# Performance work log

Hardware: AMD Instinct MI355X
Metric: run time of the kernel (lower is better)

Reference implementation:

```python
import jax, jax.numpy as jnp
import numpy as np

HIDDEN = 1024
HEADS = 16


def rotate_half(x):
    x1, x2 = jnp.split(x, 2, axis=-1)
    return jnp.concatenate((-x2, x1), axis=-1)


def rope_tables(seq_len, dim):
    inv_freq = 1.0 / 10000 ** (jnp.arange(0, dim, 2, dtype=jnp.float32) / dim)
    t = jnp.arange(seq_len, dtype=jnp.float32)
    freqs = jnp.outer(t, inv_freq)
    emb = jnp.concatenate((freqs, freqs), axis=-1)  # [S, dim]
    return jnp.cos(emb), jnp.sin(emb)


def setup_inputs() -> dict:
    key = jax.random.key(0)
    ks = jax.random.split(key, 10)
    B, S, D = 2, 2048, HIDDEN
    scale = 1.0 / np.sqrt(D)
    inp = {
        "inputs": jax.random.normal(ks[0], (B, S, D), jnp.float32),
        "context": jax.random.normal(ks[1], (B, S, D), jnp.float32),
        "Wq": jax.random.normal(ks[2], (D, D), jnp.float32) * scale,
        "bq": jnp.zeros((D,), jnp.float32),
        "Wk": jax.random.normal(ks[3], (D, D), jnp.float32) * scale,
        "bk": jnp.zeros((D,), jnp.float32),
        "Wv": jax.random.normal(ks[4], (D, D), jnp.float32) * scale,
        "bv": jnp.zeros((D,), jnp.float32),
        "Wo": jax.random.normal(ks[5], (D, D), jnp.float32) * scale,
        "bo": jnp.zeros((D,), jnp.float32),
    }
    return inp


def reference(inputs, context, Wq, bq, Wk, bk, Wv, bv, Wo, bo):
    B, S, D = inputs.shape
    H = HEADS
    hd = D // H

    q = inputs @ Wq + bq          # [B,S,D]
    k = context @ Wk + bk
    v = context @ Wv + bv

    # RoPE applied over the FULL hidden dim, pre-head-split (faithful to source).
    cos, sin = rope_tables(S, D)  # [S,D]
    # source indexes [0] after broadcasting with [1,1,S,D] tables -> effectively same values
    q = q * cos + rotate_half(q) * sin
    k = k * cos + rotate_half(k) * sin

    q = q.reshape(B, S, H, hd)
    k = k.reshape(B, S, H, hd)
    v = v.reshape(B, S, H, hd)

    # Faithful: NO transpose before attention; matmul contracts last dims of
    # q [B,S,H,hd] with k^T [B,S,hd,H] -> scores [B,S,H,H]
    scores = jnp.einsum('bshd,btd->bsht', q, jnp.zeros((1, 1, 1))) if False else None
    scores = jnp.matmul(q, jnp.swapaxes(k, -2, -1)) / jnp.sqrt(jnp.float32(hd))  # [B,S,H,H]
    attn = jax.nn.softmax(scores, axis=-1)
    ctx = jnp.matmul(attn, v)     # [B,S,H,hd]

    # source: transpose(0,2,1,3) then reshape back to (B,S,D)
    ctx = ctx.transpose(0, 2, 1, 3).reshape(B, S, D)
    out = ctx @ Wo + bo
    return out, attn
```

## Files before the change

kernel.cpp:

```cpp
#include <hip/hip_runtime.h>
#include <hip/hip_bf16.h>
#include <cstdint>

typedef __attribute__((ext_vector_type(8))) short short8;
typedef __attribute__((ext_vector_type(4))) float f32x4;
typedef __attribute__((ext_vector_type(2))) float f32x2;
typedef __attribute__((ext_vector_type(4))) float float4v;
typedef __attribute__((ext_vector_type(4))) unsigned short us4;

#define HD 1024
#define SEQ 2048

__device__ __forceinline__ unsigned short f2bf(float f) {
  uint32_t u = __builtin_bit_cast(uint32_t, f);
  return (unsigned short)((u + 0x7FFFu + ((u >> 16) & 1u)) >> 16);
}
__device__ __forceinline__ float bf2f(unsigned short s) {
  return __builtin_bit_cast(float, (uint32_t)s << 16);
}

__device__ __forceinline__ void gload16(const unsigned short* g, unsigned short* l) {
  __builtin_amdgcn_global_load_lds(
      (const __attribute__((address_space(1))) void*)g,
      (__attribute__((address_space(3))) void*)l, 16, 0, 0);
}

__global__ __launch_bounds__(256) void prep(
    const float* __restrict__ X, const float* __restrict__ Y,
    const float* __restrict__ w0, const float* __restrict__ w1,
    const float* __restrict__ w2, const float* __restrict__ w3,
    unsigned short* __restrict__ Xh, unsigned short* __restrict__ Yh,
    unsigned short* __restrict__ wt, float* __restrict__ outz,
    f32x2* __restrict__ tab) {
  __shared__ float tile[32][33];
  int bx = blockIdx.x;
  int tid = threadIdx.x;
  if (bx < 4096) {
    const float* src = (bx >= 2048) ? Y : X;
    unsigned short* oh = (bx >= 2048) ? Yh : Xh;
    int i0 = (bx & 2047) * 512 + tid;
#pragma unroll
    for (int r = 0; r < 2; ++r) {
      int i = i0 + r * 256;
      float4v v = ((const float4v*)src)[i];
      us4 h;
#pragma unroll
      for (int j = 0; j < 4; ++j) h[j] = f2bf(v[j]);
      ((us4*)oh)[i] = h;
    }
  } else if (bx < 8192) {
    int t = bx - 4096;
    int z = t >> 10;
    int rem = t & 1023;
    int bxx = rem & 31, byy = rem >> 5;
    const float* in = (z == 0) ? w0 : (z == 1) ? w1 : (z == 2) ? w2 : w3;
    unsigned short* oh = wt + (size_t)z * 1024 * 1024;
    int tx = tid & 31, ty = tid >> 5;
    int x = bxx * 32 + tx;
    int y0 = byy * 32;
    for (int i = ty; i < 32; i += 8)
      tile[i][tx] = in[(size_t)(y0 + i) * HD + x];
    __syncthreads();
    int x2 = y0 + tx;
    int y2 = bxx * 32;
    for (int i = ty; i < 32; i += 8)
      oh[(size_t)(y2 + i) * HD + x2] = f2bf(tile[tx][i]);
  } else if (bx < 9216) {
    int i0 = (bx - 8192) * 1024 + tid;
    float4v zv = {0.f, 0.f, 0.f, 0.f};
#pragma unroll
    for (int r = 0; r < 4; ++r)
      ((float4v*)outz)[i0 + r * 256] = zv;
  } else {
    int e0 = (bx - 9216) * 1024 + tid;
#pragma unroll
    for (int r = 0; r < 4; ++r) {
      int e = e0 + r * 256;
      int s = e >> 9, d = e & 511;
      float f = exp2f(-(float)d * 0.025952563241307517f);
      float th = (float)s * f;
      float sv, cv;
      sincosf(th, &sv, &cv);
      f32x2 cs; cs[0] = cv; cs[1] = sv;
      tab[e] = cs;
    }
  }
}

__global__ __launch_bounds__(256, 3) void gemm_qkv(
    const unsigned short* __restrict__ Ih, const unsigned short* __restrict__ Ch,
    const unsigned short* __restrict__ wt,
    const float* __restrict__ bq, const float* __restrict__ bk, const float* __restrict__ bv,
    unsigned short* __restrict__ qo, unsigned short* __restrict__ ko,
    unsigned short* __restrict__ vo) {
  __shared__ __align__(16) unsigned short lds[2][128][64];
  const int K = HD, N = HD;
  const size_t P = (size_t)1024 * 1024;
  int z  = blockIdx.z;
  const unsigned short* Ah = z ? Ch : Ih;
  const unsigned short* Bth = wt + (size_t)z * P;
  const float* bias = (z == 0) ? bq : (z == 1) ? bk : bv;
  unsigned short* C = (z == 0) ? qo : (z == 1) ? ko : vo;

  int m0 = blockIdx.x * 128;
  int n0 = blockIdx.y * 128;
  int tid  = threadIdx.x;
  int lane = tid & 63;
  int w    = tid >> 6;
  int quad = lane >> 4;
  int l16  = lane & 15;
  int wm = (w >> 1) * 64;
  int wn = (w & 1) * 64;

  int ro = lane >> 3;
  int sl = lane & 7;
  int ge = sl ^ (ro >> 1);
  int go = ge ^ 4;
  const unsigned short* spA_e = Ah  + (size_t)(m0 + ro) * K + ge * 8;
  const unsigned short* spA_o = Ah  + (size_t)(m0 + ro) * K + go * 8;
  const unsigned short* spB_e = Bth + (size_t)(n0 + ro) * K + ge * 8;
  const unsigned short* spB_o = Bth + (size_t)(n0 + ro) * K + go * 8;

  f32x4 acc[4][4];
#pragma unroll
  for (int t = 0; t < 4; ++t)
#pragma unroll
    for (int u = 0; u < 4; ++u) acc[t][u] = (f32x4){0.f, 0.f, 0.f, 0.f};

  for (int k0 = 0; k0 < K; k0 += 64) {
    __syncthreads();
#pragma unroll
    for (int i = 0; i < 4; ++i) {
      int seg = w + i * 4;
      const unsigned short* pa = (seg & 1) ? spA_o : spA_e;
      const unsigned short* pb = (seg & 1) ? spB_o : spB_e;
      gload16(pa + (size_t)seg * 8 * K + k0, &lds[0][seg * 8][0]);
      gload16(pb + (size_t)seg * 8 * K + k0, &lds[1][seg * 8][0]);
    }
    __syncthreads();

#pragma unroll
    for (int j = 0; j < 2; ++j) {
      int sl8 = (((j << 2) | quad) ^ (l16 >> 1)) * 8;
      short8 ah[4], bh[4];
#pragma unroll
      for (int t = 0; t < 4; ++t)
        ah[t] = *(const short8*)&lds[0][wm + t * 16 + l16][sl8];
#pragma unroll
      for (int u = 0; u < 4; ++u)
        bh[u] = *(const short8*)&lds[1][wn + u * 16 + l16][sl8];
#pragma unroll
      for (int t = 0; t < 4; ++t)
#pragma unroll
        for (int u = 0; u < 4; ++u)
          acc[t][u] = __builtin_amdgcn_mfma_f32_16x16x32_bf16(ah[t], bh[u], acc[t][u], 0, 0, 0);
    }
  }

#pragma unroll
  for (int t = 0; t < 4; ++t) {
    int row = m0 + wm + t * 16 + quad * 4;
#pragma unroll
    for (int u = 0; u < 4; ++u) {
      int col = n0 + wn + u * 16 + l16;
      float bvv = bias[col];
#pragma unroll
      for (int i = 0; i < 4; ++i)
        C[(size_t)(row + i) * N + col] = f2bf(acc[t][u][i] + bvv);
    }
  }
}

__global__ __launch_bounds__(256, 3) void gemm_o_splitk(
    const unsigned short* __restrict__ Ah, const unsigned short* __restrict__ Bth,
    const float* __restrict__ bias, float* __restrict__ C) {
  __shared__ __align__(16) unsigned short lds[2][128][64];
  const int K = HD, N = HD;
  int z  = blockIdx.z;
  int m0 = blockIdx.x * 128;
  int n0 = blockIdx.y * 128;
  int tid  = threadIdx.x;
  int lane = tid & 63;
  int w    = tid >> 6;
  int quad = lane >> 4;
  int l16  = lane & 15;
  int wm = (w >> 1) * 64;
  int wn = (w & 1) * 64;

  int ro = lane >> 3;
  int sl = lane & 7;
  int ge = sl ^ (ro >> 1);
  int go = ge ^ 4;
  const unsigned short* spA_e = Ah  + (size_t)(m0 + ro) * K + ge * 8;
  const unsigned short* spA_o = Ah  + (size_t)(m0 + ro) * K + go * 8;
  const unsigned short* spB_e = Bth + (size_t)(n0 + ro) * K + ge * 8;
  const unsigned short* spB_o = Bth + (size_t)(n0 + ro) * K + go * 8;

  f32x4 acc[4][4];
#pragma unroll
  for (int t = 0; t < 4; ++t)
#pragma unroll
    for (int u = 0; u < 4; ++u) acc[t][u] = (f32x4){0.f, 0.f, 0.f, 0.f};

  int kend = z * 512 + 512;
  for (int k0 = z * 512; k0 < kend; k0 += 64) {
    __syncthreads();
#pragma unroll
    for (int i = 0; i < 4; ++i) {
      int seg = w + i * 4;
      const unsigned short* pa = (seg & 1) ? spA_o : spA_e;
      const unsigned short* pb = (seg & 1) ? spB_o : spB_e;
      gload16(pa + (size_t)seg * 8 * K + k0, &lds[0][seg * 8][0]);
      gload16(pb + (size_t)seg * 8 * K + k0, &lds[1][seg * 8][0]);
    }
    __syncthreads();

#pragma unroll
    for (int j = 0; j < 2; ++j) {
      int sl8 = (((j << 2) | quad) ^ (l16 >> 1)) * 8;
      short8 ah[4], bh[4];
#pragma unroll
      for (int t = 0; t < 4; ++t)
        ah[t] = *(const short8*)&lds[0][wm + t * 16 + l16][sl8];
#pragma unroll
      for (int u = 0; u < 4; ++u)
        bh[u] = *(const short8*)&lds[1][wn + u * 16 + l16][sl8];
#pragma unroll
      for (int t = 0; t < 4; ++t)
#pragma unroll
        for (int u = 0; u < 4; ++u)
          acc[t][u] = __builtin_amdgcn_mfma_f32_16x16x32_bf16(ah[t], bh[u], acc[t][u], 0, 0, 0);
    }
  }

#pragma unroll
  for (int t = 0; t < 4; ++t) {
    int row = m0 + wm + t * 16 + quad * 4;
#pragma unroll
    for (int u = 0; u < 4; ++u) {
      int col = n0 + wn + u * 16 + l16;
      float bvv = (z == 0) ? bias[col] : 0.f;
#pragma unroll
      for (int i = 0; i < 4; ++i)
        atomicAdd(&C[(size_t)(row + i) * N + col], acc[t][u][i] + bvv);
    }
  }
}

__global__ __launch_bounds__(256) void attn_rope_k(
    const unsigned short* __restrict__ q, const unsigned short* __restrict__ kk,
    const unsigned short* __restrict__ v, const f32x2* __restrict__ tab,
    float* __restrict__ attn_out, unsigned short* __restrict__ ctx_h) {
  __shared__ float qs[16][68], ks[16][68], vs[16][68], as[16][17];
  int m = blockIdx.x;
  int tid = threadIdx.x;
  int s = m & (SEQ - 1);
  size_t base4 = (size_t)m * (HD / 4);
  {
    int h = tid >> 4, dd = (tid & 15) * 4;
    us4 qv = ((const us4*)q)[base4 + tid];
    us4 kv = ((const us4*)kk)[base4 + tid];
    us4 vv = ((const us4*)v)[base4 + tid];
#pragma unroll
    for (int j = 0; j < 4; ++j) {
      qs[h][dd + j] = bf2f(qv[j]);
      ks[h][dd + j] = bf2f(kv[j]);
      vs[h][dd + j] = bf2f(vv[j]);
    }
  }
  __syncthreads();
#pragma unroll
  for (int d = tid; d < 512; d += 256) {
    f32x2 cs = tab[(s << 9) + d];
    float cv = cs[0], sv = cs[1];
    int h1 = d >> 6, dd = d & 63, h2 = h1 + 8;
    float q1 = qs[h1][dd], q2 = qs[h2][dd];
    qs[h1][dd] = q1 * cv - q2 * sv;
    qs[h2][dd] = q2 * cv + q1 * sv;
    float k1 = ks[h1][dd], k2 = ks[h2][dd];
    ks[h1][dd] = k1 * cv - k2 * sv;
    ks[h2][dd] = k2 * cv + k1 * sv;
  }
  __syncthreads();
  int h = tid >> 4, t = tid & 15;
  float sc = 0.f;
#pragma unroll
  for (int d = 0; d < 64; ++d) sc = fmaf(qs[h][d], ks[t][d], sc);
  sc *= 0.125f;
  float mx = sc;
  mx = fmaxf(mx, __shfl_xor(mx, 1));
  mx = fmaxf(mx, __shfl_xor(mx, 2));
  mx = fmaxf(mx, __shfl_xor(mx, 4));
  mx = fmaxf(mx, __shfl_xor(mx, 8));
  float e = expf(sc - mx);
  float sum = e;
  sum += __shfl_xor(sum, 1);
  sum += __shfl_xor(sum, 2);
  sum += __shfl_xor(sum, 4);
  sum += __shfl_xor(sum, 8);
  float a = e / sum;
  attn_out[(size_t)m * 256 + tid] = a;
  as[h][t] = a;
  __syncthreads();
  int b = m >> 11;
  for (int j = tid; j < 1024; j += 256) {
    int h2 = j >> 6, d = j & 63;
    float c = 0.f;
#pragma unroll
    for (int t2 = 0; t2 < 16; ++t2) c = fmaf(as[h2][t2], vs[t2][d], c);
    int row = b * SEQ + h2 * 128 + (s >> 4);
    int col = (s & 15) * 64 + d;
    ctx_h[(size_t)row * HD + col] = f2bf(c);
  }
}

extern "C" void kernel_launch(void* const* d_in, const int* in_sizes, int n_in,
                              void* d_out, int out_size, void* d_ws, size_t ws_size,
                              hipStream_t stream) {
  const float* inputs  = (const float*)d_in[0];
  const float* context = (const float*)d_in[1];
  const float* Wq = (const float*)d_in[2];
  const float* bq = (const float*)d_in[3];
  const float* Wk = (const float*)d_in[4];
  const float* bk = (const float*)d_in[5];
  const float* Wv = (const float*)d_in[6];
  const float* bv = (const float*)d_in[7];
  const float* Wo = (const float*)d_in[8];
  const float* bo = (const float*)d_in[9];

  float* out  = (float*)d_out;
  float* attn = out + (size_t)4096 * 1024;

  const size_t MB = 1ull << 20;
  char* wsb = (char*)d_ws;
  unsigned short* q  = (unsigned short*)(wsb + 0 * MB);
  unsigned short* k  = (unsigned short*)(wsb + 8 * MB);
  unsigned short* v  = (unsigned short*)(wsb + 16 * MB);
  unsigned short* wt = (unsigned short*)(wsb + 24 * MB);
  unsigned short* Ih = (unsigned short*)(wsb + 32 * MB);
  unsigned short* Ch = (unsigned short*)(wsb + 40 * MB);
  f32x2* tab = (f32x2*)(wsb + 48 * MB);
  unsigned short* ctxh = Ih;

  prep<<<10240, 256, 0, stream>>>(inputs, context, Wq, Wk, Wv, Wo,
                                  Ih, Ch, wt, out, tab);

  gemm_qkv<<<dim3(32, 8, 3), 256, 0, stream>>>(Ih, Ch, wt, bq, bk, bv, q, k, v);

  attn_rope_k<<<4096, 256, 0, stream>>>(q, k, v, tab, attn, ctxh);

  const size_t P = (size_t)1024 * 1024;
  gemm_o_splitk<<<dim3(32, 8, 2), 256, 0, stream>>>(ctxh, wt + 3 * P, bo, out);
}
```

Measured before the change: 189.4 us.

## Replace split-K atomic output GEMM with 128x64 tiled direct-store GEMM

The output projection drops its two-way split-K with atomic float adds and uses narrower 128x64 tiles that cover the full K range, storing results directly. This removes the zero-fill pass over the output in the prep kernel and the atomic read-modify-write traffic. The grid stays at 512 blocks, but each block now runs twice as many K iterations on half the N width, so per-block A-tile reuse drops.

Result: faster. 170.9 us (-9.8%).

```diff
diff --git a/kernel.cpp b/kernel.cpp
--- a/kernel.cpp
+++ b/kernel.cpp
@@ -30,8 +30,7 @@
     const float* __restrict__ w0, const float* __restrict__ w1,
     const float* __restrict__ w2, const float* __restrict__ w3,
     unsigned short* __restrict__ Xh, unsigned short* __restrict__ Yh,
-    unsigned short* __restrict__ wt, float* __restrict__ outz,
-    f32x2* __restrict__ tab) {
+    unsigned short* __restrict__ wt, f32x2* __restrict__ tab) {
   __shared__ float tile[32][33];
   int bx = blockIdx.x;
   int tid = threadIdx.x;
@@ -65,14 +64,8 @@
     int y2 = bxx * 32;
     for (int i = ty; i < 32; i += 8)
       oh[(size_t)(y2 + i) * HD + x2] = f2bf(tile[tx][i]);
-  } else if (bx < 9216) {
-    int i0 = (bx - 8192) * 1024 + tid;
-    float4v zv = {0.f, 0.f, 0.f, 0.f};
-#pragma unroll
-    for (int r = 0; r < 4; ++r)
-      ((float4v*)outz)[i0 + r * 256] = zv;
   } else {
-    int e0 = (bx - 9216) * 1024 + tid;
+    int e0 = (bx - 8192) * 1024 + tid;
 #pragma unroll
     for (int r = 0; r < 4; ++r) {
       int e = e0 + r * 256;
@@ -171,21 +164,21 @@
   }
 }
 
-__global__ __launch_bounds__(256, 3) void gemm_o_splitk(
+__global__ __launch_bounds__(256, 3) void gemm_o(
     const unsigned short* __restrict__ Ah, const unsigned short* __restrict__ Bth,
     const float* __restrict__ bias, float* __restrict__ C) {
-  __shared__ __align__(16) unsigned short lds[2][128][64];
+  __shared__ __align__(16) unsigned short ldsA[128][64];
+  __shared__ __align__(16) unsigned short ldsB[64][64];
   const int K = HD, N = HD;
-  int z  = blockIdx.z;
   int m0 = blockIdx.x * 128;
-  int n0 = blockIdx.y * 128;
+  int n0 = blockIdx.y * 64;
   int tid  = threadIdx.x;
   int lane = tid & 63;
   int w    = tid >> 6;
   int quad = lane >> 4;
   int l16  = lane & 15;
   int wm = (w >> 1) * 64;
-  int wn = (w & 1) * 64;
+  int wn = (w & 1) * 32;
 
   int ro = lane >> 3;
   int sl = lane & 7;
@@ -196,39 +189,42 @@
   const unsigned short* spB_e = Bth + (size_t)(n0 + ro) * K + ge * 8;
   const unsigned short* spB_o = Bth + (size_t)(n0 + ro) * K + go * 8;
 
-  f32x4 acc[4][4];
+  f32x4 acc[4][2];
 #pragma unroll
   for (int t = 0; t < 4; ++t)
 #pragma unroll
-    for (int u = 0; u < 4; ++u) acc[t][u] = (f32x4){0.f, 0.f, 0.f, 0.f};
-
-  int kend = z * 512 + 512;
-  for (int k0 = z * 512; k0 < kend; k0 += 64) {
+    for (int u = 0; u < 2; ++u) acc[t][u] = (f32x4){0.f, 0.f, 0.f, 0.f};
+
+  for (int k0 = 0; k0 < K; k0 += 64) {
     __syncthreads();
 #pragma unroll
     for (int i = 0; i < 4; ++i) {
       int seg = w + i * 4;
       const unsigned short* pa = (seg & 1) ? spA_o : spA_e;
+      gload16(pa + (size_t)seg * 8 * K + k0, &ldsA[seg * 8][0]);
+    }
+#pragma unroll
+    for (int i = 0; i < 2; ++i) {
+      int seg = w + i * 4;
       const unsigned short* pb = (seg & 1) ? spB_o : spB_e;
-      gload16(pa + (size_t)seg * 8 * K + k0, &lds[0][seg * 8][0]);
-      gload16(pb + (size_t)seg * 8 * K + k0, &lds[1][seg * 8][0]);
+      gload16(pb + (size_t)seg * 8 * K + k0, &ldsB[seg * 8][0]);
     }
     __syncthreads();
 
 #pragma unroll
     for (int j = 0; j < 2; ++j) {
       int sl8 = (((j << 2) | quad) ^ (l16 >> 1)) * 8;
-      short8 ah[4], bh[4];
+      short8 ah[4], bh[2];
 #pragma unroll
       for (int t = 0; t < 4; ++t)
-        ah[t] = *(const short8*)&lds[0][wm + t * 16 + l16][sl8];
-#pragma unroll
-      for (int u = 0; u < 4; ++u)
-        bh[u] = *(const short8*)&lds[1][wn + u * 16 + l16][sl8];
+        ah[t] = *(const short8*)&ldsA[wm + t * 16 + l16][sl8];
+#pragma unroll
+      for (int u = 0; u < 2; ++u)
+        bh[u] = *(const short8*)&ldsB[wn + u * 16 + l16][sl8];
 #pragma unroll
       for (int t = 0; t < 4; ++t)
 #pragma unroll
-        for (int u = 0; u < 4; ++u)
+        for (int u = 0; u < 2; ++u)
           acc[t][u] = __builtin_amdgcn_mfma_f32_16x16x32_bf16(ah[t], bh[u], acc[t][u], 0, 0, 0);
     }
   }
@@ -237,12 +233,12 @@
   for (int t = 0; t < 4; ++t) {
     int row = m0 + wm + t * 16 + quad * 4;
 #pragma unroll
-    for (int u = 0; u < 4; ++u) {
+    for (int u = 0; u < 2; ++u) {
       int col = n0 + wn + u * 16 + l16;
-      float bvv = (z == 0) ? bias[col] : 0.f;
+      float bvv = bias[col];
 #pragma unroll
       for (int i = 0; i < 4; ++i)
-        atomicAdd(&C[(size_t)(row + i) * N + col], acc[t][u][i] + bvv);
+        C[(size_t)(row + i) * N + col] = acc[t][u][i] + bvv;
     }
   }
 }
@@ -342,13 +338,12 @@
   f32x2* tab = (f32x2*)(wsb + 48 * MB);
   unsigned short* ctxh = Ih;
 
-  prep<<<10240, 256, 0, stream>>>(inputs, context, Wq, Wk, Wv, Wo,
-                                  Ih, Ch, wt, out, tab);
+  prep<<<9216, 256, 0, stream>>>(inputs, context, Wq, Wk, Wv, Wo, Ih, Ch, wt, tab);
 
   gemm_qkv<<<dim3(32, 8, 3), 256, 0, stream>>>(Ih, Ch, wt, bq, bk, bv, q, k, v);
 
   attn_rope_k<<<4096, 256, 0, stream>>>(q, k, v, tab, attn, ctxh);
 
   const size_t P = (size_t)1024 * 1024;
-  gemm_o_splitk<<<dim3(32, 8, 2), 256, 0, stream>>>(ctxh, wt + 3 * P, bo, out);
-}
+  gemm_o<<<dim3(32, 16), 256, 0, stream>>>(ctxh, wt + 3 * P, bo, out);
+}
```
